# Kernel optimization log

Hardware: AMD Instinct MI355X
Metric: run time of the kernel (lower is better)

The kernel has to match this reference:

```python
import jax, jax.numpy as jnp
import numpy as np

# NF4 (NormalFloat4) codebook from QLoRA / bitsandbytes
NF4_TABLE = jnp.array([
    -1.0, -0.6961928009986877, -0.5250730514526367, -0.39491748809814453,
    -0.28444138169288635, -0.18477343022823334, -0.09105003625154495, 0.0,
    0.07958029955625534, 0.16093020141124725, 0.24611230194568634,
    0.33791524171829224, 0.44070982933044434, 0.5626170039176941,
    0.7229568362236023, 1.0], dtype=jnp.float32)

IN_FEATURES = 4096
OUT_FEATURES = 11008
BLOCKSIZE = 64
NUMEL = IN_FEATURES * OUT_FEATURES          # 45_088_768
PACKED = NUMEL // 2                          # 22_544_384
NBLOCKS = NUMEL // BLOCKSIZE                 # 704_512


def setup_inputs() -> dict:
    key = jax.random.key(0)
    k1, k2, k3, k4 = jax.random.split(key, 4)
    x = jax.random.normal(k1, (2048, IN_FEATURES), dtype=jnp.float32)
    # packed uint8 codes, stored as int32 in [0, 256)
    packed = jax.random.randint(k2, (PACKED,), 0, 256, dtype=jnp.int32)
    # per-block absmax scales (positive)
    absmax = jax.random.uniform(k3, (NBLOCKS,), dtype=jnp.float32, minval=0.01, maxval=1.0)
    bias = jax.random.normal(k4, (OUT_FEATURES,), dtype=jnp.float32)
    return {"x": x, "packed": packed, "absmax": absmax, "bias": bias}


def _dequantize_nf4(packed, absmax):
    # unpack two 4-bit codes per byte: high nibble first, then low nibble
    hi = packed >> 4            # [P]
    lo = packed & 0xF           # [P]
    codes = jnp.stack([hi, lo], axis=-1).reshape(-1)       # [numel]
    vals = jnp.take(NF4_TABLE, codes)                      # [numel]
    # per-block absmax scaling
    w = (vals.reshape(-1, BLOCKSIZE) * absmax[:, None]).reshape(OUT_FEATURES, IN_FEATURES)
    return w


def reference(x, packed, absmax, bias):
    w = _dequantize_nf4(packed, absmax)                    # [out, in]
    # y = x @ W^T + b
    return jnp.einsum('ti,oi->to', x, w) + bias[None, :]
```

## Files before the change

### kernel.cpp

```cpp
#include <hip/hip_runtime.h>
#include <hip/hip_bf16.h>


#define IN_F   4096
#define OUT_F  11008
#define M_ROWS 2048
#define BM 128
#define BN 128
#define BK 64
#define LDSS 72

typedef short  s16x8 __attribute__((ext_vector_type(8)));
typedef unsigned short u16x8 __attribute__((ext_vector_type(8)));
typedef float  f32x4 __attribute__((ext_vector_type(4)));
typedef int    i32x4 __attribute__((ext_vector_type(4)));
typedef unsigned int u32x4 __attribute__((ext_vector_type(4)));

__device__ const float NF4_C[16] = {
    -1.0f, -0.6961928009986877f, -0.5250730514526367f, -0.39491748809814453f,
    -0.28444138169288635f, -0.18477343022823334f, -0.09105003625154495f, 0.0f,
    0.07958029955625534f, 0.16093020141124725f, 0.24611230194568634f,
    0.33791524171829224f, 0.44070982933044434f, 0.5626170039176941f,
    0.7229568362236023f, 1.0f};

static __device__ __forceinline__ unsigned short f2bf(float f) {
    union { float f; unsigned int u; } c;
    c.f = f;
    unsigned int u = c.u;
    u += 0x7fffu + ((u >> 16) & 1u);
    return (unsigned short)(u >> 16);
}

static __device__ __forceinline__ void gload_lds16(const void* g, void* l) {
    __builtin_amdgcn_global_load_lds(
        (const __attribute__((address_space(1))) void*)g,
        (__attribute__((address_space(3))) void*)l, 16, 0, 0);
}

#define DQ_UNITS 5636096UL
#define CV_PAIRS 1048576UL
#define PREP_DQ_BLOCKS 1600
#define PREP_CV_BLOCKS 448

static __device__ __forceinline__ void dq_unit(i32x4 v, float s,
                                               const float2* tab,
                                               unsigned short* __restrict__ wb,
                                               size_t u) {
    unsigned int ow[4];
#pragma unroll
    for (int j = 0; j < 4; ++j) {
        const float2 t = tab[v[j] & 0xFF];
        ow[j] = (unsigned int)f2bf(t.x * s)
              | ((unsigned int)f2bf(t.y * s) << 16);
    }
    *(reinterpret_cast<u32x4*>(wb) + u) = (u32x4){ow[0], ow[1], ow[2], ow[3]};
}

__global__ __launch_bounds__(256)
void prep_kernel(const float* __restrict__ x,
                 const int* __restrict__ packed,
                 const float* __restrict__ absmax,
                 unsigned short* __restrict__ xb,
                 unsigned short* __restrict__ wb) {
    if (blockIdx.x < PREP_DQ_BLOCKS) {
        __shared__ float2 tab[256];
        tab[threadIdx.x] = make_float2(NF4_C[threadIdx.x >> 4],
                                       NF4_C[threadIdx.x & 15]);
        __syncthreads();

        const i32x4* pv = reinterpret_cast<const i32x4*>(packed);
        const size_t stride = (size_t)PREP_DQ_BLOCKS * 256;
        size_t u = (size_t)blockIdx.x * 256 + threadIdx.x;
        for (; u + stride < DQ_UNITS; u += 2 * stride) {
            const size_t u1 = u + stride;
            const i32x4 v0 = pv[u];
            const i32x4 v1 = pv[u1];
            const float s0 = absmax[u >> 3];
            const float s1 = absmax[u1 >> 3];
            dq_unit(v0, s0, tab, wb, u);
            dq_unit(v1, s1, tab, wb, u1);
        }
        if (u < DQ_UNITS) {
            const i32x4 v0 = pv[u];
            dq_unit(v0, absmax[u >> 3], tab, wb, u);
        }
    } else {
        const f32x4* xv = reinterpret_cast<const f32x4*>(x);
        const size_t stride = (size_t)PREP_CV_BLOCKS * 256;
        size_t p = (size_t)(blockIdx.x - PREP_DQ_BLOCKS) * 256 + threadIdx.x;
        for (; p < CV_PAIRS; p += stride) {
            const f32x4 a = xv[2 * p];
            const f32x4 b = xv[2 * p + 1];
            u16x8 o;
            o[0] = f2bf(a[0]); o[1] = f2bf(a[1]); o[2] = f2bf(a[2]); o[3] = f2bf(a[3]);
            o[4] = f2bf(b[0]); o[5] = f2bf(b[1]); o[6] = f2bf(b[2]); o[7] = f2bf(b[3]);
            *(reinterpret_cast<u16x8*>(xb) + p) = o;
        }
    }
}

__global__ __launch_bounds__(256, 2)
void gemm_bt_kernel(const unsigned short* __restrict__ xb,
                    const unsigned short* __restrict__ wb,
                    const float* __restrict__ bias,
                    float* __restrict__ out) {
    __shared__ __align__(16) unsigned short As[BM * BK];
    __shared__ __align__(16) unsigned short Bs[BN * BK];

    const int tid  = threadIdx.x;
    const int lane = tid & 63;
    const int wave = tid >> 6;
    const int quad = lane >> 4;
    const int l16  = lane & 15;
    const int wm = wave & 1;
    const int wn = wave >> 1;

    const int mBase = blockIdx.x * BM;
    const int nBase = blockIdx.y * BN;

    const int srow = tid >> 3;
    const int sc   = tid & 7;
    const int scS  = sc ^ (srow & 7);

    f32x4 acc[4][4];
#pragma unroll
    for (int mi = 0; mi < 4; ++mi)
#pragma unroll
        for (int ni = 0; ni < 4; ++ni)
            acc[mi][ni] = (f32x4){0.f, 0.f, 0.f, 0.f};

    const unsigned short* aSrc = xb + (size_t)(mBase + srow) * IN_F + scS * 8;
    const unsigned short* bSrc = wb + (size_t)(nBase + srow) * IN_F + scS * 8;

    const int sw = l16 & 7;

    for (int kt = 0; kt < IN_F / BK; ++kt) {
        const int k0 = kt * BK;
        __syncthreads();
#pragma unroll
        for (int i = 0; i < 4; ++i)
            gload_lds16(aSrc + (size_t)i * 32 * IN_F + k0, &As[(i * 32 + srow) * BK + sc * 8]);
#pragma unroll
        for (int i = 0; i < 4; ++i)
            gload_lds16(bSrc + (size_t)i * 32 * IN_F + k0, &Bs[(i * 32 + srow) * BK + sc * 8]);
        __syncthreads();

#pragma unroll
        for (int kk = 0; kk < 2; ++kk) {
            const int q  = kk * 4 + quad;
            const int rd = (q ^ sw) * 8;
            s16x8 af[4], bfr[4];
#pragma unroll
            for (int mi = 0; mi < 4; ++mi)
                af[mi] = *reinterpret_cast<const s16x8*>(
                    &As[(wm * 64 + mi * 16 + l16) * BK + rd]);
#pragma unroll
            for (int ni = 0; ni < 4; ++ni)
                bfr[ni] = *reinterpret_cast<const s16x8*>(
                    &Bs[(wn * 64 + ni * 16 + l16) * BK + rd]);
#pragma unroll
            for (int mi = 0; mi < 4; ++mi)
#pragma unroll
                for (int ni = 0; ni < 4; ++ni)
                    acc[mi][ni] = __builtin_amdgcn_mfma_f32_16x16x32_bf16(
                        af[mi], bfr[ni], acc[mi][ni], 0, 0, 0);
        }
    }

    float bv[4];
#pragma unroll
    for (int ni = 0; ni < 4; ++ni)
        bv[ni] = bias[nBase + wn * 64 + ni * 16 + l16];
#pragma unroll
    for (int mi = 0; mi < 4; ++mi) {
        const int rbase = mBase + wm * 64 + mi * 16 + quad * 4;
#pragma unroll
        for (int ni = 0; ni < 4; ++ni) {
            const int col = nBase + wn * 64 + ni * 16 + l16;
#pragma unroll
            for (int r = 0; r < 4; ++r)
                __builtin_nontemporal_store(acc[mi][ni][r] + bv[ni],
                    &out[(size_t)(rbase + r) * OUT_F + col]);
        }
    }
}

__global__ __launch_bounds__(256, 2)
void nf4_linear_fused(const float* __restrict__ x,
                      const int* __restrict__ packed,
                      const float* __restrict__ absmax,
                      const float* __restrict__ bias,
                      float* __restrict__ out) {
    __shared__ __align__(16) unsigned short As[BM * LDSS];
    __shared__ __align__(16) unsigned short Bs[BN * LDSS];
    __shared__ float2 tab[256];

    const int tid  = threadIdx.x;
    const int lane = tid & 63;
    const int wave = tid >> 6;
    const int quad = lane >> 4;
    const int l16  = lane & 15;
    const int wm = wave & 1;
    const int wn = wave >> 1;
    const int mBase = blockIdx.y * BM;
    const int nBase = blockIdx.x * BN;

    tab[tid] = make_float2(NF4_C[tid >> 4], NF4_C[tid & 15]);

    f32x4 acc[4][4];
#pragma unroll
    for (int mi = 0; mi < 4; ++mi)
#pragma unroll
        for (int ni = 0; ni < 4; ++ni)
            acc[mi][ni] = (f32x4){0.f, 0.f, 0.f, 0.f};

    const int brow  = tid >> 1;
    const int bhalf = tid & 1;
    const int ng    = nBase + brow;

    for (int kt = 0; kt < IN_F / BK; ++kt) {
        const int k0 = kt * BK;
        __syncthreads();
#pragma unroll
        for (int i = 0; i < 4; ++i) {
            int gid = tid + i * 256;
            int row = gid >> 3;
            int c8  = gid & 7;
            const float4* src = reinterpret_cast<const float4*>(
                x + (size_t)(mBase + row) * IN_F + k0 + c8 * 8);
            float4 v0 = src[0];
            float4 v1 = src[1];
            u16x8 o;
            o[0] = f2bf(v0.x); o[1] = f2bf(v0.y); o[2] = f2bf(v0.z); o[3] = f2bf(v0.w);
            o[4] = f2bf(v1.x); o[5] = f2bf(v1.y); o[6] = f2bf(v1.z); o[7] = f2bf(v1.w);
            *reinterpret_cast<u16x8*>(&As[row * LDSS + c8 * 8]) = o;
        }
        {
            const float scale = absmax[(size_t)ng * 64 + (k0 >> 6)];
            const int4* bp = reinterpret_cast<const int4*>(
                packed + (size_t)ng * (IN_F / 2) + (k0 >> 1) + bhalf * 16);
            const int colw = bhalf * 32;
#pragma unroll
            for (int c = 0; c < 4; ++c) {
                int4 v = bp[c];
                int vs[4] = {v.x, v.y, v.z, v.w};
                unsigned int ow[4];
#pragma unroll
                for (int j = 0; j < 4; ++j) {
                    float2 t = tab[vs[j] & 0xFF];
                    ow[j] = (unsigned int)f2bf(t.x * scale)
                          | ((unsigned int)f2bf(t.y * scale) << 16);
                }
                *reinterpret_cast<uint4*>(&Bs[brow * LDSS + colw + c * 8]) =
                    *reinterpret_cast<const uint4*>(ow);
            }
        }
        __syncthreads();

#pragma unroll
        for (int kk = 0; kk < 2; ++kk) {
            const int kof = kk * 32 + quad * 8;
            s16x8 af[4], bfr[4];
#pragma unroll
            for (int mi = 0; mi < 4; ++mi)
                af[mi] = *reinterpret_cast<const s16x8*>(
                    &As[(wm * 64 + mi * 16 + l16) * LDSS + kof]);
#pragma unroll
            for (int ni = 0; ni < 4; ++ni)
                bfr[ni] = *reinterpret_cast<const s16x8*>(
                    &Bs[(wn * 64 + ni * 16 + l16) * LDSS + kof]);
#pragma unroll
            for (int mi = 0; mi < 4; ++mi)
#pragma unroll
                for (int ni = 0; ni < 4; ++ni)
                    acc[mi][ni] = __builtin_amdgcn_mfma_f32_16x16x32_bf16(
                        af[mi], bfr[ni], acc[mi][ni], 0, 0, 0);
        }
    }

    float bv[4];
#pragma unroll
    for (int ni = 0; ni < 4; ++ni)
        bv[ni] = bias[nBase + wn * 64 + ni * 16 + l16];
#pragma unroll
    for (int mi = 0; mi < 4; ++mi) {
        const int rbase = mBase + wm * 64 + mi * 16 + quad * 4;
#pragma unroll
        for (int ni = 0; ni < 4; ++ni) {
            const int col = nBase + wn * 64 + ni * 16 + l16;
#pragma unroll
            for (int r = 0; r < 4; ++r)
                out[(size_t)(rbase + r) * OUT_F + col] = acc[mi][ni][r] + bv[ni];
        }
    }
}

extern "C" void kernel_launch(void* const* d_in, const int* in_sizes, int n_in,
                              void* d_out, int out_size, void* d_ws, size_t ws_size,
                              hipStream_t stream) {
    const float* x      = (const float*)d_in[0];
    const int*   packed = (const int*)d_in[1];
    const float* absmax = (const float*)d_in[2];
    const float* bias   = (const float*)d_in[3];
    float* out = (float*)d_out;

    const size_t xb_bytes = (size_t)M_ROWS * IN_F * 2;
    const size_t wb_bytes = (size_t)OUT_F * IN_F * 2;
    if (ws_size >= xb_bytes + wb_bytes) {
        unsigned short* xb = (unsigned short*)d_ws;
        unsigned short* wb = (unsigned short*)((char*)d_ws + xb_bytes);
        prep_kernel<<<dim3(PREP_DQ_BLOCKS + PREP_CV_BLOCKS), dim3(256), 0, stream>>>(
            x, packed, absmax, xb, wb);
        gemm_bt_kernel<<<dim3(M_ROWS / BM, OUT_F / BN), dim3(256), 0, stream>>>(
            xb, wb, bias, out);
    } else {
        nf4_linear_fused<<<dim3(OUT_F / BN, M_ROWS / BM), dim3(256), 0, stream>>>(
            x, packed, absmax, bias, out);
    }
}
```

Baseline: 374.9 us.

## Fuse NF4 dequantization into GEMM B-tile loading with register prefetch

Drops the separate dequantization pass that wrote a full bf16 weight matrix to workspace. The GEMM now reads packed NF4 codes and absmax per tile, dequantizes them through an LDS lookup table, and writes the bf16 B tile into swizzled LDS. The next tile's packed codes are prefetched into registers. This removes the large bf16 weight write and re-read, but every M-block (16 per weight tile) now repeats the dequant arithmetic inside the GEMM main loop, adding VALU work and register pressure there.

```diff
diff --git a/kernel.cpp b/kernel.cpp
--- a/kernel.cpp
+++ b/kernel.cpp
@@ -37,77 +37,37 @@
         (__attribute__((address_space(3))) void*)l, 16, 0, 0);
 }
 
-#define DQ_UNITS 5636096UL
 #define CV_PAIRS 1048576UL
-#define PREP_DQ_BLOCKS 1600
-#define PREP_CV_BLOCKS 448
-
-static __device__ __forceinline__ void dq_unit(i32x4 v, float s,
-                                               const float2* tab,
-                                               unsigned short* __restrict__ wb,
-                                               size_t u) {
-    unsigned int ow[4];
-#pragma unroll
-    for (int j = 0; j < 4; ++j) {
-        const float2 t = tab[v[j] & 0xFF];
-        ow[j] = (unsigned int)f2bf(t.x * s)
-              | ((unsigned int)f2bf(t.y * s) << 16);
-    }
-    *(reinterpret_cast<u32x4*>(wb) + u) = (u32x4){ow[0], ow[1], ow[2], ow[3]};
-}
+#define PREP_CV_BLOCKS 1024
 
 __global__ __launch_bounds__(256)
-void prep_kernel(const float* __restrict__ x,
-                 const int* __restrict__ packed,
-                 const float* __restrict__ absmax,
-                 unsigned short* __restrict__ xb,
-                 unsigned short* __restrict__ wb) {
-    if (blockIdx.x < PREP_DQ_BLOCKS) {
-        __shared__ float2 tab[256];
-        tab[threadIdx.x] = make_float2(NF4_C[threadIdx.x >> 4],
-                                       NF4_C[threadIdx.x & 15]);
-        __syncthreads();
-
-        const i32x4* pv = reinterpret_cast<const i32x4*>(packed);
-        const size_t stride = (size_t)PREP_DQ_BLOCKS * 256;
-        size_t u = (size_t)blockIdx.x * 256 + threadIdx.x;
-        for (; u + stride < DQ_UNITS; u += 2 * stride) {
-            const size_t u1 = u + stride;
-            const i32x4 v0 = pv[u];
-            const i32x4 v1 = pv[u1];
-            const float s0 = absmax[u >> 3];
-            const float s1 = absmax[u1 >> 3];
-            dq_unit(v0, s0, tab, wb, u);
-            dq_unit(v1, s1, tab, wb, u1);
-        }
-        if (u < DQ_UNITS) {
-            const i32x4 v0 = pv[u];
-            dq_unit(v0, absmax[u >> 3], tab, wb, u);
-        }
-    } else {
-        const f32x4* xv = reinterpret_cast<const f32x4*>(x);
-        const size_t stride = (size_t)PREP_CV_BLOCKS * 256;
-        size_t p = (size_t)(blockIdx.x - PREP_DQ_BLOCKS) * 256 + threadIdx.x;
-        for (; p < CV_PAIRS; p += stride) {
-            const f32x4 a = xv[2 * p];
-            const f32x4 b = xv[2 * p + 1];
-            u16x8 o;
-            o[0] = f2bf(a[0]); o[1] = f2bf(a[1]); o[2] = f2bf(a[2]); o[3] = f2bf(a[3]);
-            o[4] = f2bf(b[0]); o[5] = f2bf(b[1]); o[6] = f2bf(b[2]); o[7] = f2bf(b[3]);
-            *(reinterpret_cast<u16x8*>(xb) + p) = o;
-        }
+void prep_x_kernel(const float* __restrict__ x, unsigned short* __restrict__ xb) {
+    const f32x4* xv = reinterpret_cast<const f32x4*>(x);
+    const size_t stride = (size_t)PREP_CV_BLOCKS * 256;
+    size_t p = (size_t)blockIdx.x * 256 + threadIdx.x;
+    for (; p < CV_PAIRS; p += stride) {
+        const f32x4 a = xv[2 * p];
+        const f32x4 b = xv[2 * p + 1];
+        u16x8 o;
+        o[0] = f2bf(a[0]); o[1] = f2bf(a[1]); o[2] = f2bf(a[2]); o[3] = f2bf(a[3]);
+        o[4] = f2bf(b[0]); o[5] = f2bf(b[1]); o[6] = f2bf(b[2]); o[7] = f2bf(b[3]);
+        *(reinterpret_cast<u16x8*>(xb) + p) = o;
     }
 }
 
 __global__ __launch_bounds__(256, 2)
-void gemm_bt_kernel(const unsigned short* __restrict__ xb,
-                    const unsigned short* __restrict__ wb,
-                    const float* __restrict__ bias,
-                    float* __restrict__ out) {
+void gemm_fused_kernel(const unsigned short* __restrict__ xb,
+                       const int* __restrict__ packed,
+                       const float* __restrict__ absmax,
+                       const float* __restrict__ bias,
+                       float* __restrict__ out) {
     __shared__ __align__(16) unsigned short As[BM * BK];
     __shared__ __align__(16) unsigned short Bs[BN * BK];
+    __shared__ float2 tab[256];
 
     const int tid  = threadIdx.x;
+    tab[tid] = make_float2(NF4_C[tid >> 4], NF4_C[tid & 15]);
+
     const int lane = tid & 63;
     const int wave = tid >> 6;
     const int quad = lane >> 4;
@@ -121,6 +81,20 @@
     const int srow = tid >> 3;
     const int sc   = tid & 7;
     const int scS  = sc ^ (srow & 7);
+    const unsigned short* aSrc = xb + (size_t)(mBase + srow) * IN_F + scS * 8;
+
+    const int brow  = tid >> 1;
+    const int bhalf = tid & 1;
+    const int ng    = nBase + brow;
+    const i32x4* pbase = reinterpret_cast<const i32x4*>(packed)
+                         + (size_t)ng * 512 + bhalf * 4;
+    const float* smax = absmax + (size_t)ng * 64;
+    unsigned short* bDst[4];
+#pragma unroll
+    for (int j = 0; j < 4; ++j) {
+        const int c = bhalf * 4 + j;
+        bDst[j] = &Bs[brow * BK + ((c ^ (brow & 7)) * 8)];
+    }
 
     f32x4 acc[4][4];
 #pragma unroll
@@ -129,20 +103,36 @@
         for (int ni = 0; ni < 4; ++ni)
             acc[mi][ni] = (f32x4){0.f, 0.f, 0.f, 0.f};
 
-    const unsigned short* aSrc = xb + (size_t)(mBase + srow) * IN_F + scS * 8;
-    const unsigned short* bSrc = wb + (size_t)(nBase + srow) * IN_F + scS * 8;
-
     const int sw = l16 & 7;
+
+    i32x4 pk[4];
+    float bs0 = smax[0];
+#pragma unroll
+    for (int j = 0; j < 4; ++j) pk[j] = pbase[j];
 
     for (int kt = 0; kt < IN_F / BK; ++kt) {
         const int k0 = kt * BK;
         __syncthreads();
 #pragma unroll
         for (int i = 0; i < 4; ++i)
-            gload_lds16(aSrc + (size_t)i * 32 * IN_F + k0, &As[(i * 32 + srow) * BK + sc * 8]);
-#pragma unroll
-        for (int i = 0; i < 4; ++i)
-            gload_lds16(bSrc + (size_t)i * 32 * IN_F + k0, &Bs[(i * 32 + srow) * BK + sc * 8]);
+            gload_lds16(aSrc + (size_t)i * 32 * IN_F + k0,
+                        &As[(i * 32 + srow) * BK + sc * 8]);
+        const int ktn = (kt < IN_F / BK - 1) ? kt + 1 : kt;
+        i32x4 nk[4];
+#pragma unroll
+        for (int j = 0; j < 4; ++j) nk[j] = pbase[ktn * 8 + j];
+        const float bsn = smax[ktn];
+#pragma unroll
+        for (int j = 0; j < 4; ++j) {
+            unsigned int ow[4];
+#pragma unroll
+            for (int e = 0; e < 4; ++e) {
+                const float2 t = tab[pk[j][e] & 0xFF];
+                ow[e] = (unsigned int)f2bf(t.x * bs0)
+                      | ((unsigned int)f2bf(t.y * bs0) << 16);
+            }
+            *reinterpret_cast<u32x4*>(bDst[j]) = (u32x4){ow[0], ow[1], ow[2], ow[3]};
+        }
         __syncthreads();
 
 #pragma unroll
@@ -165,6 +155,9 @@
                     acc[mi][ni] = __builtin_amdgcn_mfma_f32_16x16x32_bf16(
                         af[mi], bfr[ni], acc[mi][ni], 0, 0, 0);
         }
+#pragma unroll
+        for (int j = 0; j < 4; ++j) pk[j] = nk[j];
+        bs0 = bsn;
     }
 
     float bv[4];
@@ -305,14 +298,11 @@
     float* out = (float*)d_out;
 
     const size_t xb_bytes = (size_t)M_ROWS * IN_F * 2;
-    const size_t wb_bytes = (size_t)OUT_F * IN_F * 2;
-    if (ws_size >= xb_bytes + wb_bytes) {
+    if (ws_size >= xb_bytes) {
         unsigned short* xb = (unsigned short*)d_ws;
-        unsigned short* wb = (unsigned short*)((char*)d_ws + xb_bytes);
-        prep_kernel<<<dim3(PREP_DQ_BLOCKS + PREP_CV_BLOCKS), dim3(256), 0, stream>>>(
-            x, packed, absmax, xb, wb);
-        gemm_bt_kernel<<<dim3(M_ROWS / BM, OUT_F / BN), dim3(256), 0, stream>>>(
-            xb, wb, bias, out);
+        prep_x_kernel<<<dim3(PREP_CV_BLOCKS), dim3(256), 0, stream>>>(x, xb);
+        gemm_fused_kernel<<<dim3(M_ROWS / BM, OUT_F / BN), dim3(256), 0, stream>>>(
+            xb, packed, absmax, bias, out);
     } else {
         nf4_linear_fused<<<dim3(OUT_F / BN, M_ROWS / BM), dim3(256), 0, stream>>>(
             x, packed, absmax, bias, out);
```

After: 455.5 us. 1.21x slower.
